# Kernel optimization log

Measured on AMD Instinct MI355X. Metric: run time of the kernel, lower is better.

The kernel has to match this reference:

```python
import jax, jax.numpy as jnp
import numpy as np

N = 8192      # atoms
E = 4096      # edges (become transformer tokens)
E2 = 65536    # edges of second graph y
VOCAB = 119
DE = 200      # node_features == embedding_dim
D = 256
H = 8
L = 2
DFF = 2048


def _bn(x, g, b, eps=1e-6):
    m = x.mean(0)
    v = x.var(0)
    return (x - m) * jax.lax.rsqrt(v + eps) * g + b


def _ln(x, g, b, eps=1e-5):
    m = x.mean(-1, keepdims=True)
    v = ((x - m) ** 2).mean(-1, keepdims=True)
    return (x - m) * jax.lax.rsqrt(v + eps) * g + b


def _gcn(x, ei, W, b):
    # PyG GCNConv: add self loops, symmetric deg^-1/2 normalization
    n = x.shape[0]
    loop = jnp.arange(n)
    src = jnp.concatenate([ei[0], loop])
    dst = jnp.concatenate([ei[1], loop])
    deg = jax.ops.segment_sum(jnp.ones(src.shape[0], x.dtype), dst, num_segments=n)
    dinv = jnp.where(deg > 0, jax.lax.rsqrt(jnp.maximum(deg, 1e-12)), 0.0)
    msg = (x @ W)[src] * (dinv[src] * dinv[dst])[:, None]
    return jax.ops.segment_sum(msg, dst, num_segments=n) + b


def _mha(x, wi, bi, wo, bo):
    S, d = x.shape
    dh = d // H
    q, k, v = jnp.split(x @ wi + bi, 3, axis=1)
    q = q.reshape(S, H, dh)
    k = k.reshape(S, H, dh)
    v = v.reshape(S, H, dh)
    sc = jnp.einsum('qhd,khd->hqk', q, k) * (1.0 / np.sqrt(dh))
    a = jax.nn.softmax(sc, axis=-1)
    o = jnp.einsum('hqk,khd->qhd', a, v).reshape(S, d)
    return o @ wo + bo


def setup_inputs() -> dict:
    key = jax.random.key(0)
    ks = iter(jax.random.split(key, 64))
    nrm = lambda shape, s=0.05: jax.random.normal(next(ks), shape, jnp.float32) * s
    d = {}
    d['x'] = jax.random.randint(next(ks), (N,), 0, VOCAB)
    d['edge_index'] = jax.random.randint(next(ks), (2, E), 1, N + 1)  # 1-based, code subtracts 1
    d['pos'] = jax.random.normal(next(ks), (N, 3), jnp.float32)
    d['y'] = jax.random.randint(next(ks), (2, E2), 0, E)
    d['emb'] = nrm((VOCAB, DE), 1.0)
    d['fc1_w'] = nrm((1, DE))
    d['fc1_b'] = jnp.zeros((DE,), jnp.float32)
    d['bn4_g'] = jnp.ones((DE,), jnp.float32)
    d['bn4_b'] = jnp.zeros((DE,), jnp.float32)
    d['conv1_w'] = nrm((DE, D))
    d['conv1_b'] = jnp.zeros((D,), jnp.float32)
    d['conv2_w'] = nrm((D, D))
    d['conv2_b'] = jnp.zeros((D,), jnp.float32)
    for i in (1, 2, 3):
        d['bn%d_g' % i] = jnp.ones((D,), jnp.float32)
        d['bn%d_b' % i] = jnp.zeros((D,), jnp.float32)
    d['in_proj_w'] = nrm((L, D, 3 * D))
    d['in_proj_b'] = jnp.zeros((L, 3 * D), jnp.float32)
    d['out_proj_w'] = nrm((L, D, D))
    d['out_proj_b'] = jnp.zeros((L, D), jnp.float32)
    d['ln1_g'] = jnp.ones((L, D), jnp.float32)
    d['ln1_b'] = jnp.zeros((L, D), jnp.float32)
    d['ln2_g'] = jnp.ones((L, D), jnp.float32)
    d['ln2_b'] = jnp.zeros((L, D), jnp.float32)
    d['ff1_w'] = nrm((L, D, DFF))
    d['ff1_b'] = jnp.zeros((L, DFF), jnp.float32)
    d['ff2_w'] = nrm((L, DFF, D))
    d['ff2_b'] = jnp.zeros((L, D), jnp.float32)
    d['fc3_w'] = nrm((D, 1))
    d['fc3_b'] = jnp.zeros((1,), jnp.float32)
    d['fc4_w'] = nrm((D, 9))
    d['fc4_b'] = jnp.zeros((9,), jnp.float32)
    return d


def reference(x, edge_index, pos, y, emb, fc1_w, fc1_b, bn4_g, bn4_b,
              conv1_w, conv1_b, conv2_w, conv2_b,
              bn1_g, bn1_b, bn2_g, bn2_b, bn3_g, bn3_b,
              in_proj_w, in_proj_b, out_proj_w, out_proj_b,
              ln1_g, ln1_b, ln2_g, ln2_b, ff1_w, ff1_b, ff2_w, ff2_b,
              fc3_w, fc3_b, fc4_w, fc4_b):
    h = emb[x]                                   # [N, DE]
    ei = edge_index - 1
    row, col = ei[0], ei[1]
    ef = jnp.linalg.norm(pos[col] - pos[row], axis=1, keepdims=True)  # [E,1]
    ef = _bn(ef @ fc1_w + fc1_b, bn4_g, bn4_b)   # [E, DE]
    h = h[row] + h[col] + ef                     # [E, DE] edges -> tokens
    h = jax.nn.leaky_relu(_gcn(h, y, conv1_w, conv1_b))
    h = _bn(h, bn1_g, bn1_b)
    h = jax.nn.leaky_relu(h + _gcn(h, y, conv2_w, conv2_b))
    h = _bn(h, bn2_g, bn2_b)
    # post-norm TransformerEncoder (unbatched seq of length E), dropout=0
    for i in range(L):
        h = _ln(h + _mha(h, in_proj_w[i], in_proj_b[i], out_proj_w[i], out_proj_b[i]),
                ln1_g[i], ln1_b[i])
        ff = jax.nn.relu(h @ ff1_w[i] + ff1_b[i]) @ ff2_w[i] + ff2_b[i]
        h = _ln(h + ff, ln2_g[i], ln2_b[i])
    h = jax.nn.leaky_relu(h)
    h = _bn(h, bn3_g, bn3_b)
    sym_out = h @ fc3_w + fc3_b
    asym_out = h @ fc4_w + fc4_b
    return (sym_out, asym_out)
```

## Files before the change

kernel.cpp:

```cpp
#include <hip/hip_runtime.h>
#include <math.h>

#define ETOK 4096
#define NE2  65536
#define DEF  200
#define DM   256
#define NH   8
#define DH   32
#define DFFN 2048
#define NKS  4

#define QSCALE_LOG2E 0.25503474f

typedef __attribute__((ext_vector_type(8))) short bfrag8;
typedef __attribute__((ext_vector_type(4))) float f32x4;
typedef __attribute__((ext_vector_type(4))) short short4v;

__device__ __forceinline__ unsigned short f2bf(float f) {
  union { float f; unsigned u; } v; v.f = f;
  unsigned u = v.u + 0x7fffu + ((v.u >> 16) & 1u);
  return (unsigned short)(u >> 16);
}
__device__ __forceinline__ float bf2f(unsigned short u) {
  union { unsigned u; float f; } v;
  v.u = ((unsigned)u) << 16;
  return v.f;
}
__device__ __forceinline__ unsigned cvt_pk_bf16(float lo, float hi) {
  unsigned r;
  asm("v_cvt_pk_bf16_f32 %0, %1, %2" : "=v"(r) : "v"(lo), "v"(hi));
  return r;
}

__device__ __forceinline__ float wave_sum(float v) {
#pragma unroll
  for (int off = 32; off > 0; off >>= 1) v += __shfl_xor(v, off);
  return v;
}
__device__ __forceinline__ float block_sum(float v, float* red) {
  v = wave_sum(v);
  int lane = threadIdx.x & 63, w = threadIdx.x >> 6;
  if (lane == 0) red[w] = v;
  __syncthreads();
  float t = red[0] + red[1] + red[2] + red[3];
  __syncthreads();
  return t;
}

__global__ void edge_deg_kernel(const int* __restrict__ ei, const float* __restrict__ pos,
                                float* __restrict__ ef0, float* __restrict__ stats,
                                const int* __restrict__ y, int* __restrict__ deg) {
  __shared__ float red[4];
  int e2 = blockIdx.x * 256 + threadIdx.x;
  atomicAdd(&deg[y[NE2 + e2]], 1);
  if (blockIdx.x < 16) {
    int e = blockIdx.x * 256 + threadIdx.x;
    int r = ei[e] - 1;
    int c = ei[ETOK + e] - 1;
    float dx = pos[c * 3 + 0] - pos[r * 3 + 0];
    float dy = pos[c * 3 + 1] - pos[r * 3 + 1];
    float dz = pos[c * 3 + 2] - pos[r * 3 + 2];
    float d = sqrtf(dx * dx + dy * dy + dz * dz);
    ef0[e] = d;
    float s = block_sum(d, red);
    float s2 = block_sum(d * d, red);
    if (threadIdx.x == 0) {
      atomicAdd(stats + 0, s);
      atomicAdd(stats + 1, s2);
    }
  }
}

__global__ void token_build_kernel(const int* __restrict__ x, const int* __restrict__ ei,
                                   const float* __restrict__ emb, const float* __restrict__ fc1_w,
                                   const float* __restrict__ bn4_g, const float* __restrict__ bn4_b,
                                   const float* __restrict__ ef0, const float* __restrict__ stats,
                                   unsigned short* __restrict__ tokbf) {
  int e = blockIdx.x;
  int j = threadIdx.x;
  float m = stats[0] * (1.0f / 4096.0f);
  float v = stats[1] * (1.0f / 4096.0f) - m * m;
  int xr = x[ei[e] - 1];
  int xc = x[ei[ETOK + e] - 1];
  float dd = ef0[e] - m;
  float val = 0.f;
  if (j < DEF) {
    float w = fc1_w[j];
    float s = w * rsqrtf(v * w * w + 1e-6f) * bn4_g[j];
    val = emb[(size_t)xr * DEF + j] + emb[(size_t)xc * DEF + j] + dd * s + bn4_b[j];
  }
  tokbf[(size_t)e * 256 + j] = f2bf(val);
}

__global__ void scan_kernel(const int* __restrict__ deg, int* __restrict__ off,
                            int* __restrict__ cursor, float* __restrict__ dinv) {
  __shared__ int part[256];
  int t = threadIdx.x;
  int v[16];
  int s = 0;
#pragma unroll
  for (int i = 0; i < 16; ++i) {
    v[i] = deg[t * 16 + i];
    s += v[i];
  }
  part[t] = s;
  __syncthreads();
  if (t == 0) {
    int a = 0;
#pragma unroll 1
    for (int i = 0; i < 256; ++i) {
      int tmp = part[i];
      part[i] = a;
      a += tmp;
    }
    off[4096] = a;
  }
  __syncthreads();
  int a = part[t];
#pragma unroll
  for (int i = 0; i < 16; ++i) {
    off[t * 16 + i] = a;
    cursor[t * 16 + i] = a;
    dinv[t * 16 + i] = rsqrtf((float)(v[i] + 1));
    a += v[i];
  }
}
__global__ void fill_kernel(const int* __restrict__ y, int* __restrict__ cursor,
                            int* __restrict__ srcl) {
  int e = blockIdx.x * 256 + threadIdx.x;
  int s = y[e];
  int d = y[NE2 + e];
  int slot = atomicAdd(&cursor[d], 1);
  srcl[slot] = s;
}

template <int RES, int ACT>
__global__ __launch_bounds__(256) void gather_kernel(const float* __restrict__ xw,
                                                     const int* __restrict__ off,
                                                     const int* __restrict__ srcl,
                                                     const float* __restrict__ dinv,
                                                     const float* __restrict__ bias,
                                                     const float* __restrict__ resid,
                                                     float* __restrict__ out) {
  __shared__ int slds[256];
  __shared__ float dlds[256];
  const int d = blockIdx.x;
  const int c = threadIdx.x;
  const int b0 = off[d], b1 = off[d + 1];
  const float dd = dinv[d];
  float acc = 0.f;
  for (int base = b0; base < b1; base += 256) {
    int n = min(256, b1 - base);
    __syncthreads();
    if (c < n) {
      int s = srcl[base + c];
      slds[c] = s;
      dlds[c] = dinv[s];
    }
    __syncthreads();
    for (int j = 0; j < n; ++j) {
      int s = slds[j];
      acc = fmaf(xw[(size_t)s * DM + c], dlds[j], acc);
    }
  }
  size_t idx = (size_t)d * DM + c;
  float v = bias[c] + xw[idx] * dd * dd + acc * dd;
  if (RES) v += resid[idx];
  if (ACT) v = v > 0.f ? v : 0.01f * v;
  out[idx] = v;
}

struct WEntry {
  const float* src;
  unsigned short* dst;
  int K, N, KP, tilesN, ntiles;
};
struct WPack {
  WEntry e[10];
};
__global__ __launch_bounds__(256) void wtrans_all_kernel(WPack p) {
  __shared__ float tl[32][33];
  int t = blockIdx.x;
  int i = 0;
  while (t >= p.e[i].ntiles) {
    t -= p.e[i].ntiles;
    ++i;
  }
  const WEntry w = p.e[i];
  int nb = (t % w.tilesN) * 32;
  int kb = (t / w.tilesN) * 32;
  int tx = threadIdx.x & 31, ty = threadIdx.x >> 5;
#pragma unroll
  for (int r = ty; r < 32; r += 8) {
    int k = kb + r, n = nb + tx;
    tl[r][tx] = (k < w.K && n < w.N) ? w.src[(size_t)k * w.N + n] : 0.f;
  }
  __syncthreads();
#pragma unroll
  for (int r = ty; r < 32; r += 8) {
    int n = nb + r, k = kb + tx;
    if (n < w.N) w.dst[(size_t)n * w.KP + k] = f2bf(tl[tx][r]);
  }
}

template <int BM, int BN, int OUTBF, int ACT, int QS>
__global__ __launch_bounds__(256) void mfma_gemm(const unsigned short* __restrict__ A,
                                                 const unsigned short* __restrict__ Bt,
                                                 const float* __restrict__ bias,
                                                 void* __restrict__ Cout, int M, int N, int K) {
  constexpr int BK = 64;
  constexpr int TM = BM / 32, TN = BN / 32;
  constexpr int ACH = BM / 32, BCH = BN / 32;
  __shared__ unsigned short Alds[BM * BK];
  __shared__ unsigned short Blds[BN * BK];
  const int tid = threadIdx.x;
  const int lane = tid & 63, wid = tid >> 6;
  const int g = lane >> 4, q = lane & 15;
  const int wr = wid >> 1, wc = wid & 1;
  const int m0 = blockIdx.y * BM, n0 = blockIdx.x * BN;

  f32x4 acc[TM][TN];
#pragma unroll
  for (int i = 0; i < TM; ++i)
#pragma unroll
    for (int j = 0; j < TN; ++j) acc[i][j] = (f32x4){0.f, 0.f, 0.f, 0.f};

  for (int k0 = 0; k0 < K; k0 += BK) {
    __syncthreads();
#pragma unroll
    for (int c = 0; c < ACH; ++c) {
      int chunk = wid * ACH + c;
      int row = chunk * 8 + (lane >> 3);
      int cb = ((lane & 7) * 16) ^ ((row & 7) << 4);
      const char* gp = (const char*)A + ((size_t)(m0 + row) * K + k0) * 2 + cb;
      __builtin_amdgcn_global_load_lds(
          (const __attribute__((address_space(1))) unsigned int*)gp,
          (__attribute__((address_space(3))) unsigned int*)(Alds + chunk * 512), 16, 0, 0);
    }
#pragma unroll
    for (int c = 0; c < BCH; ++c) {
      int chunk = wid * BCH + c;
      int row = chunk * 8 + (lane >> 3);
      int cb = ((lane & 7) * 16) ^ ((row & 7) << 4);
      const char* gp = (const char*)Bt + ((size_t)(n0 + row) * K + k0) * 2 + cb;
      __builtin_amdgcn_global_load_lds(
          (const __attribute__((address_space(1))) unsigned int*)gp,
          (__attribute__((address_space(3))) unsigned int*)(Blds + chunk * 512), 16, 0, 0);
    }
    __syncthreads();
#pragma unroll
    for (int ks = 0; ks < 2; ++ks) {
      bfrag8 af[TM], bfr[TN];
#pragma unroll
      for (int mi = 0; mi < TM; ++mi) {
        int row = wr * (BM / 2) + mi * 16 + q;
        int cb = (ks * 64 + g * 16) ^ ((row & 7) << 4);
        af[mi] = *(const bfrag8*)((const char*)Alds + row * 128 + cb);
      }
#pragma unroll
      for (int ni = 0; ni < TN; ++ni) {
        int row = wc * (BN / 2) + ni * 16 + q;
        int cb = (ks * 64 + g * 16) ^ ((row & 7) << 4);
        bfr[ni] = *(const bfrag8*)((const char*)Blds + row * 128 + cb);
      }
#pragma unroll
      for (int mi = 0; mi < TM; ++mi)
#pragma unroll
        for (int ni = 0; ni < TN; ++ni)
          acc[mi][ni] = __builtin_amdgcn_mfma_f32_16x16x32_bf16(af[mi], bfr[ni], acc[mi][ni], 0, 0, 0);
    }
  }
#pragma unroll
  for (int mi = 0; mi < TM; ++mi) {
    int row = m0 + wr * (BM / 2) + mi * 16 + g * 4;
#pragma unroll
    for (int ni = 0; ni < TN; ++ni) {
      int col = n0 + wc * (BN / 2) + ni * 16 + q;
      float bv = bias ? bias[col] : 0.f;
#pragma unroll
      for (int r = 0; r < 4; ++r) {
        float v = acc[mi][ni][r] + bv;
        if (QS && col < DM) v *= QSCALE_LOG2E;
        if (ACT == 1) v = fmaxf(v, 0.f);
        if (OUTBF)
          ((unsigned short*)Cout)[(size_t)(row + r) * N + col] = f2bf(v);
        else
          ((float*)Cout)[(size_t)(row + r) * N + col] = v;
      }
    }
  }
}

template <int LEAKY>
__global__ __launch_bounds__(256) void col_accum_kernel(const float* __restrict__ x,
                                                        float* __restrict__ colm,
                                                        float* __restrict__ colv) {
  int c = threadIdx.x;
  int r0 = blockIdx.x * 16;
  float s = 0.f, s2 = 0.f;
#pragma unroll
  for (int i = 0; i < 16; ++i) {
    float v = x[(size_t)(r0 + i) * DM + c];
    if (LEAKY) v = v > 0.f ? v : 0.01f * v;
    s += v;
    s2 += v * v;
  }
  atomicAdd(&colm[c], s);
  atomicAdd(&colv[c], s2);
}
template <int LEAKY>
__global__ void bn_apply_kernel(const float* __restrict__ x, const float* __restrict__ colm,
                                const float* __restrict__ colv, const float* __restrict__ g,
                                const float* __restrict__ b, float* __restrict__ outf,
                                unsigned short* __restrict__ outb, int C) {
  size_t i = (size_t)blockIdx.x * 256 + threadIdx.x;
  int c = (int)(i % C);
  float mean = colm[c] * (1.0f / 4096.0f);
  float var = colv[c] * (1.0f / 4096.0f) - mean * mean;
  float v0 = x[i];
  if (LEAKY) v0 = v0 > 0.f ? v0 : 0.01f * v0;
  float v = (v0 - mean) * rsqrtf(var + 1e-6f) * g[c] + b[c];
  outf[i] = v;
  if (outb) outb[i] = f2bf(v);
}

__global__ __launch_bounds__(256) void attn_mfma_kernel(const unsigned short* __restrict__ qkv,
                                                        unsigned short* __restrict__ Opart,
                                                        float* __restrict__ Lpart) {
  const int h = blockIdx.y;
  const int qblk = blockIdx.x * 64;
  const int chunk = blockIdx.z;
  const int tid = threadIdx.x;
  const int wid = tid >> 6, lane = tid & 63;
  const int g = lane >> 4, q = lane & 15;

  __shared__ unsigned short Klds[2][64][40];
  __shared__ unsigned int Vtw[2][32][36];
  __shared__ unsigned short Plds[4][16][72];

  bfrag8 qfrag;
  {
    const unsigned short* qp = qkv + (size_t)(qblk + wid * 16 + q) * 768 + h * DH + g * 8;
    qfrag = *(const bfrag8*)qp;
  }
  const f32x4 zero = {0.f, 0.f, 0.f, 0.f};

  const int skey = tid >> 2;
  const int sdb = (tid & 3) * 8;
  const int kp2 = tid >> 3;
  const int dc = (tid & 7) * 4;

  const int kbeg = chunk * (ETOK / NKS);
  const int NT = (ETOK / NKS) / 64;

  const unsigned short* kptr = qkv + (size_t)(kbeg + skey) * 768 + DM + h * DH + sdb;
  const unsigned short* vptr = qkv + (size_t)(kbeg + kp2 * 2) * 768 + 2 * DM + h * DH + dc;

  bfrag8 kreg = *(const bfrag8*)kptr;
  kptr += 64 * 768;
  short4v va = *(const short4v*)vptr;
  short4v vb = *(const short4v*)(vptr + 768);
  vptr += 64 * 768;

  float lsum = 0.f;
  f32x4 o0 = zero, o1 = zero;

  for (int t = 0; t < NT; ++t) {
    const int buf = t & 1;
    *(bfrag8*)&Klds[buf][skey][sdb] = kreg;
#pragma unroll
    for (int j = 0; j < 4; ++j) {
      unsigned pkv = (unsigned)(unsigned short)va[j] | ((unsigned)(unsigned short)vb[j] << 16);
      Vtw[buf][dc + j][kp2] = pkv;
    }
    __syncthreads();
    if (t + 1 < NT) {
      kreg = *(const bfrag8*)kptr;
      kptr += 64 * 768;
      va = *(const short4v*)vptr;
      vb = *(const short4v*)(vptr + 768);
      vptr += 64 * 768;
    }

    f32x4 st[4];
    __builtin_amdgcn_s_setprio(1);
#pragma unroll
    for (int tt = 0; tt < 4; ++tt) {
      bfrag8 kf = *(const bfrag8*)&Klds[buf][tt * 16 + q][g * 8];
      st[tt] = __builtin_amdgcn_mfma_f32_16x16x32_bf16(kf, qfrag, zero, 0, 0, 0);
    }
    __builtin_amdgcn_s_setprio(0);

    float ps = 0.f;
    unsigned pk8[8];
#pragma unroll
    for (int tt = 0; tt < 4; ++tt) {
      float p0 = __builtin_exp2f(st[tt][0]);
      float p1 = __builtin_exp2f(st[tt][1]);
      float p2 = __builtin_exp2f(st[tt][2]);
      float p3 = __builtin_exp2f(st[tt][3]);
      ps += (p0 + p1) + (p2 + p3);
      pk8[tt * 2 + 0] = cvt_pk_bf16(p0, p1);
      pk8[tt * 2 + 1] = cvt_pk_bf16(p2, p3);
    }
    lsum += ps;

#pragma unroll
    for (int tt = 0; tt < 4; ++tt) {
      uint2 w2;
      w2.x = pk8[tt * 2 + 0];
      w2.y = pk8[tt * 2 + 1];
      *(uint2*)&Plds[wid][q][tt * 16 + g * 4] = w2;
    }

    __builtin_amdgcn_s_setprio(1);
#pragma unroll
    for (int kg = 0; kg < 2; ++kg) {
      bfrag8 pa = *(const bfrag8*)&Plds[wid][q][kg * 32 + g * 8];
      bfrag8 vb0 = *(const bfrag8*)&Vtw[buf][q][kg * 16 + g * 4];
      bfrag8 vb1 = *(const bfrag8*)&Vtw[buf][16 + q][kg * 16 + g * 4];
      o0 = __builtin_amdgcn_mfma_f32_16x16x32_bf16(pa, vb0, o0, 0, 0, 0);
      o1 = __builtin_amdgcn_mfma_f32_16x16x32_bf16(pa, vb1, o1, 0, 0, 0);
    }
    __builtin_amdgcn_s_setprio(0);
  }

  lsum += __shfl_xor(lsum, 16);
  lsum += __shfl_xor(lsum, 32);
#pragma unroll
  for (int r = 0; r < 4; ++r) {
    int row = qblk + wid * 16 + g * 4 + r;
    unsigned short* op = Opart + ((size_t)chunk * ETOK + row) * DM + h * DH;
    op[q] = f2bf(o0[r]);
    op[16 + q] = f2bf(o1[r]);
  }
  if (lane < 16) {
    int row = qblk + wid * 16 + lane;
    Lpart[((size_t)chunk * ETOK + row) * NH + h] = lsum;
  }
}

__global__ __launch_bounds__(256) void attn_combine_kernel(const unsigned short* __restrict__ Opart,
                                                           const float* __restrict__ Lpart,
                                                           unsigned short* __restrict__ out) {
  __shared__ float ls[NKS][NH];
  const int row = blockIdx.x;
  const int c = threadIdx.x;
  if (c < NKS * NH) {
    ls[c >> 3][c & 7] = Lpart[((size_t)(c >> 3) * ETOK + row) * NH + (c & 7)];
  }
  __syncthreads();
  const int h = c >> 5;
  float lstar = (ls[0][h] + ls[1][h]) + (ls[2][h] + ls[3][h]);
  float acc = 0.f;
#pragma unroll
  for (int ch = 0; ch < NKS; ++ch)
    acc += bf2f(Opart[((size_t)ch * ETOK + row) * DM + c]);
  out[(size_t)row * DM + c] = f2bf(acc / lstar);
}

__global__ void add_ln_kernel(const float* __restrict__ x, const float* __restrict__ r,
                              float* __restrict__ outf, unsigned short* __restrict__ outb,
                              const float* __restrict__ g, const float* __restrict__ b) {
  __shared__ float red[4];
  int row = blockIdx.x, t = threadIdx.x;
  size_t idx = (size_t)row * DM + t;
  float v = x[idx] + r[idx];
  float mean = block_sum(v, red) * (1.0f / 256.0f);
  float dv = v - mean;
  float var = block_sum(dv * dv, red) * (1.0f / 256.0f);
  float o = dv * rsqrtf(var + 1e-5f) * g[t] + b[t];
  outf[idx] = o;
  outb[idx] = f2bf(o);
}

__global__ void head_kernel(const float* __restrict__ h, const float* __restrict__ colm,
                            const float* __restrict__ colv, const float* __restrict__ bng,
                            const float* __restrict__ bnb, const float* __restrict__ fc3w,
                            const float* __restrict__ fc3b, const float* __restrict__ fc4w,
                            const float* __restrict__ fc4b, float* __restrict__ out) {
  int wave = threadIdx.x >> 6, lane = threadIdx.x & 63;
  int tok = blockIdx.x * 4 + wave;
  const float* hr = h + (size_t)tok * DM;
  float hv[4];
#pragma unroll
  for (int i = 0; i < 4; ++i) {
    int col = lane * 4 + i;
    float v = hr[col];
    v = v > 0.f ? v : 0.01f * v;
    float mean = colm[col] * (1.0f / 4096.0f);
    float var = colv[col] * (1.0f / 4096.0f) - mean * mean;
    hv[i] = (v - mean) * rsqrtf(var + 1e-6f) * bng[col] + bnb[col];
  }
  float acc = 0.f;
#pragma unroll
  for (int i = 0; i < 4; ++i) acc += hv[i] * fc3w[lane * 4 + i];
  acc = wave_sum(acc);
  if (lane == 0) out[tok] = acc + fc3b[0];
#pragma unroll
  for (int j = 0; j < 9; ++j) {
    float a = 0.f;
#pragma unroll
    for (int i = 0; i < 4; ++i) a += hv[i] * fc4w[(lane * 4 + i) * 9 + j];
    a = wave_sum(a);
    if (lane == 0) out[ETOK + (size_t)tok * 9 + j] = a + fc4b[j];
  }
}

extern "C" void kernel_launch(void* const* d_in, const int* in_sizes, int n_in,
                              void* d_out, int out_size, void* d_ws, size_t ws_size,
                              hipStream_t stream) {
  const int* x = (const int*)d_in[0];
  const int* edge_index = (const int*)d_in[1];
  const float* pos = (const float*)d_in[2];
  const int* y = (const int*)d_in[3];
  const float* emb = (const float*)d_in[4];
  const float* fc1_w = (const float*)d_in[5];
  const float* bn4_g = (const float*)d_in[7];
  const float* bn4_b = (const float*)d_in[8];
  const float* conv1_w = (const float*)d_in[9];
  const float* conv1_b = (const float*)d_in[10];
  const float* conv2_w = (const float*)d_in[11];
  const float* conv2_b = (const float*)d_in[12];
  const float* bn1_g = (const float*)d_in[13];
  const float* bn1_b = (const float*)d_in[14];
  const float* bn2_g = (const float*)d_in[15];
  const float* bn2_b = (const float*)d_in[16];
  const float* bn3_g = (const float*)d_in[17];
  const float* bn3_b = (const float*)d_in[18];
  const float* ipw = (const float*)d_in[19];
  const float* ipb = (const float*)d_in[20];
  const float* opw = (const float*)d_in[21];
  const float* opb = (const float*)d_in[22];
  const float* ln1_g = (const float*)d_in[23];
  const float* ln1_b = (const float*)d_in[24];
  const float* ln2_g = (const float*)d_in[25];
  const float* ln2_b = (const float*)d_in[26];
  const float* ff1w = (const float*)d_in[27];
  const float* ff1b = (const float*)d_in[28];
  const float* ff2w = (const float*)d_in[29];
  const float* ff2b = (const float*)d_in[30];
  const float* fc3w = (const float*)d_in[31];
  const float* fc3b = (const float*)d_in[32];
  const float* fc4w = (const float*)d_in[33];
  const float* fc4b = (const float*)d_in[34];
  float* outp = (float*)d_out;

  char* wsp = (char*)d_ws;
  auto alloc = [&](size_t bytes) {
    void* p = (void*)wsp;
    wsp += (bytes + 255) & ~(size_t)255;
    return p;
  };
  unsigned short* big_bf = (unsigned short*)alloc((size_t)ETOK * DFFN * 2);
  unsigned short* attno = (unsigned short*)alloc((size_t)ETOK * DM * 2);
  unsigned short* h_bf = (unsigned short*)alloc((size_t)ETOK * DM * 2);
  unsigned short* tok_bf = (unsigned short*)alloc((size_t)ETOK * 256 * 2);
  float* hf = (float*)alloc((size_t)ETOK * DM * 4);
  float* t1 = (float*)alloc((size_t)ETOK * DM * 4);
  float* t2 = (float*)alloc((size_t)ETOK * DM * 4);
  unsigned short* Opart = (unsigned short*)alloc((size_t)NKS * ETOK * DM * 2);
  float* Lpart = (float*)alloc((size_t)NKS * ETOK * NH * 4);
  unsigned short* c1wt = (unsigned short*)alloc(256 * 256 * 2);
  unsigned short* c2wt = (unsigned short*)alloc(256 * 256 * 2);
  unsigned short* ipwt = (unsigned short*)alloc((size_t)2 * 768 * 256 * 2);
  unsigned short* opwt = (unsigned short*)alloc((size_t)2 * 256 * 256 * 2);
  unsigned short* f1wt = (unsigned short*)alloc((size_t)2 * 2048 * 256 * 2);
  unsigned short* f2wt = (unsigned short*)alloc((size_t)2 * 256 * 2048 * 2);
  float* ef0 = (float*)alloc(ETOK * 4);
  float* dinv = (float*)alloc(ETOK * 4);
  int* off = (int*)alloc((ETOK + 1) * 4);
  int* cursor = (int*)alloc(ETOK * 4);
  int* srcl = (int*)alloc(NE2 * 4);
  char* z0 = wsp;
  float* stats = (float*)alloc(8 * 4);
  float* colm = (float*)alloc(3 * DM * 4);
  float* colv = (float*)alloc(3 * DM * 4);
  int* deg = (int*)alloc(ETOK * 4);
  size_t zlen = (char*)wsp - z0;

  hipMemsetAsync(z0, 0, zlen, stream);

  WPack wp;
  int ntot = 0;
  auto went = [&](int i, const float* src, unsigned short* dst, int K, int N, int KP) {
    wp.e[i].src = src;
    wp.e[i].dst = dst;
    wp.e[i].K = K;
    wp.e[i].N = N;
    wp.e[i].KP = KP;
    wp.e[i].tilesN = (N + 31) / 32;
    wp.e[i].ntiles = ((N + 31) / 32) * (KP / 32);
    ntot += wp.e[i].ntiles;
  };
  went(0, conv1_w, c1wt, 200, 256, 256);
  went(1, conv2_w, c2wt, 256, 256, 256);
  went(2, ipw, ipwt, 256, 768, 256);
  went(3, ipw + (size_t)256 * 768, ipwt + (size_t)768 * 256, 256, 768, 256);
  went(4, opw, opwt, 256, 256, 256);
  went(5, opw + (size_t)256 * 256, opwt + (size_t)256 * 256, 256, 256, 256);
  went(6, ff1w, f1wt, 256, 2048, 256);
  went(7, ff1w + (size_t)256 * 2048, f1wt + (size_t)2048 * 256, 256, 2048, 256);
  went(8, ff2w, f2wt, 2048, 256, 2048);
  went(9, ff2w + (size_t)2048 * 256, f2wt + (size_t)256 * 2048, 2048, 256, 2048);
  wtrans_all_kernel<<<ntot, 256, 0, stream>>>(wp);

  edge_deg_kernel<<<NE2 / 256, 256, 0, stream>>>(edge_index, pos, ef0, stats, y, deg);
  scan_kernel<<<1, 256, 0, stream>>>(deg, off, cursor, dinv);
  fill_kernel<<<NE2 / 256, 256, 0, stream>>>(y, cursor, srcl);
  token_build_kernel<<<ETOK, 256, 0, stream>>>(x, edge_index, emb, fc1_w, bn4_g, bn4_b, ef0,
                                               stats, tok_bf);

  mfma_gemm<32, 32, 0, 0, 0><<<dim3(8, 128), 256, 0, stream>>>(tok_bf, c1wt, nullptr, t1, ETOK, DM, 256);
  gather_kernel<0, 1><<<ETOK, 256, 0, stream>>>(t1, off, srcl, dinv, conv1_b, nullptr, t2);
  col_accum_kernel<0><<<ETOK / 16, 256, 0, stream>>>(t2, colm, colv);
  bn_apply_kernel<0><<<ETOK * DM / 256, 256, 0, stream>>>(t2, colm, colv, bn1_g, bn1_b, hf, h_bf, DM);

  mfma_gemm<32, 32, 0, 0, 0><<<dim3(8, 128), 256, 0, stream>>>(h_bf, c2wt, nullptr, t1, ETOK, DM, 256);
  gather_kernel<1, 1><<<ETOK, 256, 0, stream>>>(t1, off, srcl, dinv, conv2_b, hf, t2);
  col_accum_kernel<0><<<ETOK / 16, 256, 0, stream>>>(t2, colm + DM, colv + DM);
  bn_apply_kernel<0><<<ETOK * DM / 256, 256, 0, stream>>>(t2, colm + DM, colv + DM, bn2_g, bn2_b,
                                                          hf, h_bf, DM);

  for (int i = 0; i < 2; ++i) {
    mfma_gemm<32, 32, 1, 0, 1><<<dim3(24, 128), 256, 0, stream>>>(
        h_bf, ipwt + (size_t)i * 768 * 256, ipb + (size_t)i * 768, big_bf, ETOK, 768, 256);
    attn_mfma_kernel<<<dim3(ETOK / 64, NH, NKS), 256, 0, stream>>>(big_bf, Opart, Lpart);
    attn_combine_kernel<<<ETOK, 256, 0, stream>>>(Opart, Lpart, attno);
    mfma_gemm<32, 32, 0, 0, 0><<<dim3(8, 128), 256, 0, stream>>>(
        attno, opwt + (size_t)i * 256 * 256, opb + (size_t)i * DM, t2, ETOK, DM, 256);
    add_ln_kernel<<<ETOK, 256, 0, stream>>>(t2, hf, hf, h_bf, ln1_g + (size_t)i * DM,
                                            ln1_b + (size_t)i * DM);
    mfma_gemm<64, 64, 1, 1, 0><<<dim3(32, 64), 256, 0, stream>>>(
        h_bf, f1wt + (size_t)i * 2048 * 256, ff1b + (size_t)i * DFFN, big_bf, ETOK, DFFN, 256);
    mfma_gemm<32, 32, 0, 0, 0><<<dim3(8, 128), 256, 0, stream>>>(
        big_bf, f2wt + (size_t)i * 256 * 2048, ff2b + (size_t)i * DM, t2, ETOK, DM, 2048);
    add_ln_kernel<<<ETOK, 256, 0, stream>>>(t2, hf, hf, h_bf, ln2_g + (size_t)i * DM,
                                            ln2_b + (size_t)i * DM);
  }

  col_accum_kernel<1><<<ETOK / 16, 256, 0, stream>>>(hf, colm + 2 * DM, colv + 2 * DM);
  head_kernel<<<ETOK / 4, 256, 0, stream>>>(hf, colm + 2 * DM, colv + 2 * DM, bn3_g, bn3_b,
                                            fc3w, fc3b, fc4w, fc4b, outp);
}
```

Measured before the change: 343.8 us.

## Write V transposed from QKV GEMM and process 32 queries per wave in attention

The QKV projection GEMM now writes Q and K into a 512-wide buffer and V into a separate transposed buffer (head-dim major, token minor). The attention kernel can then load V tiles with a single 16-byte vector store to LDS instead of packing pairs of rows. Each wave also handles 32 query rows instead of 16, so every K/V tile staged in LDS is reused twice and half as many blocks are launched. The cost is more registers per thread (launch_bounds 256,4), a larger P buffer in LDS, and scattered 8-byte transposed stores in the GEMM epilogue.

```diff
diff --git a/kernel.cpp b/kernel.cpp
--- a/kernel.cpp
+++ b/kernel.cpp
@@ -15,6 +15,7 @@
 typedef __attribute__((ext_vector_type(8))) short bfrag8;
 typedef __attribute__((ext_vector_type(4))) float f32x4;
 typedef __attribute__((ext_vector_type(4))) short short4v;
+typedef __attribute__((ext_vector_type(4))) unsigned int u32x4;
 
 __device__ __forceinline__ unsigned short f2bf(float f) {
   union { float f; unsigned u; } v; v.f = f;
@@ -203,11 +204,12 @@
   }
 }
 
-template <int BM, int BN, int OUTBF, int ACT, int QS>
+template <int BM, int BN, int OUTBF, int ACT, int QS, int VSPLIT>
 __global__ __launch_bounds__(256) void mfma_gemm(const unsigned short* __restrict__ A,
                                                  const unsigned short* __restrict__ Bt,
                                                  const float* __restrict__ bias,
-                                                 void* __restrict__ Cout, int M, int N, int K) {
+                                                 void* __restrict__ Cout, void* __restrict__ Cout2,
+                                                 int M, int N, int K) {
   constexpr int BK = 64;
   constexpr int TM = BM / 32, TN = BN / 32;
   constexpr int ACH = BM / 32, BCH = BN / 32;
@@ -277,15 +279,22 @@
     for (int ni = 0; ni < TN; ++ni) {
       int col = n0 + wc * (BN / 2) + ni * 16 + q;
       float bv = bias ? bias[col] : 0.f;
-#pragma unroll
-      for (int r = 0; r < 4; ++r) {
-        float v = acc[mi][ni][r] + bv;
-        if (QS && col < DM) v *= QSCALE_LOG2E;
-        if (ACT == 1) v = fmaxf(v, 0.f);
-        if (OUTBF)
-          ((unsigned short*)Cout)[(size_t)(row + r) * N + col] = f2bf(v);
-        else
-          ((float*)Cout)[(size_t)(row + r) * N + col] = v;
+      if (VSPLIT && col >= 512) {
+        short4v pkv;
+#pragma unroll
+        for (int r = 0; r < 4; ++r) pkv[r] = (short)f2bf(acc[mi][ni][r] + bv);
+        *(short4v*)((unsigned short*)Cout2 + (size_t)(col - 512) * M + row) = pkv;
+      } else {
+#pragma unroll
+        for (int r = 0; r < 4; ++r) {
+          float v = acc[mi][ni][r] + bv;
+          if (QS && col < DM) v *= QSCALE_LOG2E;
+          if (ACT == 1) v = fmaxf(v, 0.f);
+          if (OUTBF)
+            ((unsigned short*)Cout)[(size_t)(row + r) * (VSPLIT ? 512 : N) + col] = f2bf(v);
+          else
+            ((float*)Cout)[(size_t)(row + r) * N + col] = v;
+        }
       }
     }
   }
@@ -324,11 +333,12 @@
   if (outb) outb[i] = f2bf(v);
 }
 
-__global__ __launch_bounds__(256) void attn_mfma_kernel(const unsigned short* __restrict__ qkv,
-                                                        unsigned short* __restrict__ Opart,
-                                                        float* __restrict__ Lpart) {
+__global__ __launch_bounds__(256, 4) void attn_mfma_kernel(const unsigned short* __restrict__ qk,
+                                                           const unsigned short* __restrict__ vt,
+                                                           unsigned short* __restrict__ Opart,
+                                                           float* __restrict__ Lpart) {
   const int h = blockIdx.y;
-  const int qblk = blockIdx.x * 64;
+  const int qblk = blockIdx.x * 128;
   const int chunk = blockIdx.z;
   const int tid = threadIdx.x;
   const int wid = tid >> 6, lane = tid & 63;
@@ -336,107 +346,123 @@
 
   __shared__ unsigned short Klds[2][64][40];
   __shared__ unsigned int Vtw[2][32][36];
-  __shared__ unsigned short Plds[4][16][72];
-
-  bfrag8 qfrag;
+  __shared__ unsigned short Plds[4][32][72];
+
+  bfrag8 qfrag0, qfrag1;
   {
-    const unsigned short* qp = qkv + (size_t)(qblk + wid * 16 + q) * 768 + h * DH + g * 8;
-    qfrag = *(const bfrag8*)qp;
+    const unsigned short* qp = qk + (size_t)(qblk + wid * 32 + q) * 512 + h * DH + g * 8;
+    qfrag0 = *(const bfrag8*)qp;
+    qfrag1 = *(const bfrag8*)(qp + 16 * 512);
   }
   const f32x4 zero = {0.f, 0.f, 0.f, 0.f};
 
   const int skey = tid >> 2;
   const int sdb = (tid & 3) * 8;
-  const int kp2 = tid >> 3;
-  const int dc = (tid & 7) * 4;
+  const int sd = tid >> 3;
+  const int sk4 = (tid & 7) * 4;
 
   const int kbeg = chunk * (ETOK / NKS);
   const int NT = (ETOK / NKS) / 64;
 
-  const unsigned short* kptr = qkv + (size_t)(kbeg + skey) * 768 + DM + h * DH + sdb;
-  const unsigned short* vptr = qkv + (size_t)(kbeg + kp2 * 2) * 768 + 2 * DM + h * DH + dc;
+  const unsigned short* kptr = qk + (size_t)(kbeg + skey) * 512 + DM + h * DH + sdb;
+  const unsigned short* vptr = vt + (size_t)(h * DH + sd) * ETOK + kbeg + sk4 * 2;
 
   bfrag8 kreg = *(const bfrag8*)kptr;
-  kptr += 64 * 768;
-  short4v va = *(const short4v*)vptr;
-  short4v vb = *(const short4v*)(vptr + 768);
-  vptr += 64 * 768;
-
-  float lsum = 0.f;
-  f32x4 o0 = zero, o1 = zero;
+  kptr += (size_t)64 * 512;
+  u32x4 vreg = *(const u32x4*)vptr;
+  vptr += 64;
+
+  float lsum0 = 0.f, lsum1 = 0.f;
+  f32x4 o00 = zero, o01 = zero, o10 = zero, o11 = zero;
 
   for (int t = 0; t < NT; ++t) {
     const int buf = t & 1;
     *(bfrag8*)&Klds[buf][skey][sdb] = kreg;
-#pragma unroll
-    for (int j = 0; j < 4; ++j) {
-      unsigned pkv = (unsigned)(unsigned short)va[j] | ((unsigned)(unsigned short)vb[j] << 16);
-      Vtw[buf][dc + j][kp2] = pkv;
-    }
+    *(u32x4*)&Vtw[buf][sd][sk4] = vreg;
     __syncthreads();
     if (t + 1 < NT) {
       kreg = *(const bfrag8*)kptr;
-      kptr += 64 * 768;
-      va = *(const short4v*)vptr;
-      vb = *(const short4v*)(vptr + 768);
-      vptr += 64 * 768;
-    }
-
-    f32x4 st[4];
+      kptr += (size_t)64 * 512;
+      vreg = *(const u32x4*)vptr;
+      vptr += 64;
+    }
+
+    f32x4 st0[4], st1[4];
     __builtin_amdgcn_s_setprio(1);
 #pragma unroll
     for (int tt = 0; tt < 4; ++tt) {
       bfrag8 kf = *(const bfrag8*)&Klds[buf][tt * 16 + q][g * 8];
-      st[tt] = __builtin_amdgcn_mfma_f32_16x16x32_bf16(kf, qfrag, zero, 0, 0, 0);
+      st0[tt] = __builtin_amdgcn_mfma_f32_16x16x32_bf16(kf, qfrag0, zero, 0, 0, 0);
+      st1[tt] = __builtin_amdgcn_mfma_f32_16x16x32_bf16(kf, qfrag1, zero, 0, 0, 0);
     }
     __builtin_amdgcn_s_setprio(0);
 
-    float ps = 0.f;
-    unsigned pk8[8];
-#pragma unroll
-    for (int tt = 0; tt < 4; ++tt) {
-      float p0 = __builtin_exp2f(st[tt][0]);
-      float p1 = __builtin_exp2f(st[tt][1]);
-      float p2 = __builtin_exp2f(st[tt][2]);
-      float p3 = __builtin_exp2f(st[tt][3]);
-      ps += (p0 + p1) + (p2 + p3);
-      pk8[tt * 2 + 0] = cvt_pk_bf16(p0, p1);
-      pk8[tt * 2 + 1] = cvt_pk_bf16(p2, p3);
-    }
-    lsum += ps;
-
-#pragma unroll
-    for (int tt = 0; tt < 4; ++tt) {
-      uint2 w2;
-      w2.x = pk8[tt * 2 + 0];
-      w2.y = pk8[tt * 2 + 1];
-      *(uint2*)&Plds[wid][q][tt * 16 + g * 4] = w2;
+    {
+      float ps = 0.f;
+#pragma unroll
+      for (int tt = 0; tt < 4; ++tt) {
+        float p0 = __builtin_exp2f(st0[tt][0]);
+        float p1 = __builtin_exp2f(st0[tt][1]);
+        float p2 = __builtin_exp2f(st0[tt][2]);
+        float p3 = __builtin_exp2f(st0[tt][3]);
+        ps += (p0 + p1) + (p2 + p3);
+        uint2 w2;
+        w2.x = cvt_pk_bf16(p0, p1);
+        w2.y = cvt_pk_bf16(p2, p3);
+        *(uint2*)&Plds[wid][q][tt * 16 + g * 4] = w2;
+      }
+      lsum0 += ps;
+    }
+    {
+      float ps = 0.f;
+#pragma unroll
+      for (int tt = 0; tt < 4; ++tt) {
+        float p0 = __builtin_exp2f(st1[tt][0]);
+        float p1 = __builtin_exp2f(st1[tt][1]);
+        float p2 = __builtin_exp2f(st1[tt][2]);
+        float p3 = __builtin_exp2f(st1[tt][3]);
+        ps += (p0 + p1) + (p2 + p3);
+        uint2 w2;
+        w2.x = cvt_pk_bf16(p0, p1);
+        w2.y = cvt_pk_bf16(p2, p3);
+        *(uint2*)&Plds[wid][16 + q][tt * 16 + g * 4] = w2;
+      }
+      lsum1 += ps;
     }
 
     __builtin_amdgcn_s_setprio(1);
 #pragma unroll
     for (int kg = 0; kg < 2; ++kg) {
-      bfrag8 pa = *(const bfrag8*)&Plds[wid][q][kg * 32 + g * 8];
       bfrag8 vb0 = *(const bfrag8*)&Vtw[buf][q][kg * 16 + g * 4];
       bfrag8 vb1 = *(const bfrag8*)&Vtw[buf][16 + q][kg * 16 + g * 4];
-      o0 = __builtin_amdgcn_mfma_f32_16x16x32_bf16(pa, vb0, o0, 0, 0, 0);
-      o1 = __builtin_amdgcn_mfma_f32_16x16x32_bf16(pa, vb1, o1, 0, 0, 0);
+      bfrag8 pa0 = *(const bfrag8*)&Plds[wid][q][kg * 32 + g * 8];
+      bfrag8 pa1 = *(const bfrag8*)&Plds[wid][16 + q][kg * 32 + g * 8];
+      o00 = __builtin_amdgcn_mfma_f32_16x16x32_bf16(pa0, vb0, o00, 0, 0, 0);
+      o01 = __builtin_amdgcn_mfma_f32_16x16x32_bf16(pa0, vb1, o01, 0, 0, 0);
+      o10 = __builtin_amdgcn_mfma_f32_16x16x32_bf16(pa1, vb0, o10, 0, 0, 0);
+      o11 = __builtin_amdgcn_mfma_f32_16x16x32_bf16(pa1, vb1, o11, 0, 0, 0);
     }
     __builtin_amdgcn_s_setprio(0);
   }
 
-  lsum += __shfl_xor(lsum, 16);
-  lsum += __shfl_xor(lsum, 32);
+  lsum0 += __shfl_xor(lsum0, 16);
+  lsum0 += __shfl_xor(lsum0, 32);
+  lsum1 += __shfl_xor(lsum1, 16);
+  lsum1 += __shfl_xor(lsum1, 32);
 #pragma unroll
   for (int r = 0; r < 4; ++r) {
-    int row = qblk + wid * 16 + g * 4 + r;
-    unsigned short* op = Opart + ((size_t)chunk * ETOK + row) * DM + h * DH;
-    op[q] = f2bf(o0[r]);
-    op[16 + q] = f2bf(o1[r]);
+    int row0 = qblk + wid * 32 + g * 4 + r;
+    unsigned short* op0 = Opart + ((size_t)chunk * ETOK + row0) * DM + h * DH;
+    op0[q] = f2bf(o00[r]);
+    op0[16 + q] = f2bf(o01[r]);
+    unsigned short* op1 = op0 + (size_t)16 * DM;
+    op1[q] = f2bf(o10[r]);
+    op1[16 + q] = f2bf(o11[r]);
   }
   if (lane < 16) {
-    int row = qblk + wid * 16 + lane;
-    Lpart[((size_t)chunk * ETOK + row) * NH + h] = lsum;
+    int row = qblk + wid * 32 + lane;
+    Lpart[((size_t)chunk * ETOK + row) * NH + h] = lsum0;
+    Lpart[((size_t)chunk * ETOK + row + 16) * NH + h] = lsum1;
   }
 }
 
@@ -553,6 +579,8 @@
     return p;
   };
   unsigned short* big_bf = (unsigned short*)alloc((size_t)ETOK * DFFN * 2);
+  unsigned short* qk_bf = (unsigned short*)alloc((size_t)ETOK * 512 * 2);
+  unsigned short* vt_bf = (unsigned short*)alloc((size_t)DM * ETOK * 2);
   unsigned short* attno = (unsigned short*)alloc((size_t)ETOK * DM * 2);
   unsigned short* h_bf = (unsigned short*)alloc((size_t)ETOK * DM * 2);
   unsigned short* tok_bf = (unsigned short*)alloc((size_t)ETOK * 256 * 2);
@@ -611,30 +639,32 @@
   token_build_kernel<<<ETOK, 256, 0, stream>>>(x, edge_index, emb, fc1_w, bn4_g, bn4_b, ef0,
                                                stats, tok_bf);
 
-  mfma_gemm<32, 32, 0, 0, 0><<<dim3(8, 128), 256, 0, stream>>>(tok_bf, c1wt, nullptr, t1, ETOK, DM, 256);
+  mfma_gemm<32, 32, 0, 0, 0, 0><<<dim3(8, 128), 256, 0, stream>>>(tok_bf, c1wt, nullptr, t1,
+                                                                  nullptr, ETOK, DM, 256);
   gather_kernel<0, 1><<<ETOK, 256, 0, stream>>>(t1, off, srcl, dinv, conv1_b, nullptr, t2);
   col_accum_kernel<0><<<ETOK / 16, 256, 0, stream>>>(t2, colm, colv);
   bn_apply_kernel<0><<<ETOK * DM / 256, 256, 0, stream>>>(t2, colm, colv, bn1_g, bn1_b, hf, h_bf, DM);
 
-  mfma_gemm<32, 32, 0, 0, 0><<<dim3(8, 128), 256, 0, stream>>>(h_bf, c2wt, nullptr, t1, ETOK, DM, 256);
+  mfma_gemm<32, 32, 0, 0, 0, 0><<<dim3(8, 128), 256, 0, stream>>>(h_bf, c2wt, nullptr, t1,
+                                                                  nullptr, ETOK, DM, 256);
   gather_kernel<1, 1><<<ETOK, 256, 0, stream>>>(t1, off, srcl, dinv, conv2_b, hf, t2);
   col_accum_kernel<0><<<ETOK / 16, 256, 0, stream>>>(t2, colm + DM, colv + DM);
   bn_apply_kernel<0><<<ETOK * DM / 256, 256, 0, stream>>>(t2, colm + DM, colv + DM, bn2_g, bn2_b,
                                                           hf, h_bf, DM);
 
   for (int i = 0; i < 2; ++i) {
-    mfma_gemm<32, 32, 1, 0, 1><<<dim3(24, 128), 256, 0, stream>>>(
-        h_bf, ipwt + (size_t)i * 768 * 256, ipb + (size_t)i * 768, big_bf, ETOK, 768, 256);
-    attn_mfma_kernel<<<dim3(ETOK / 64, NH, NKS), 256, 0, stream>>>(big_bf, Opart, Lpart);
+    mfma_gemm<32, 32, 1, 0, 1, 1><<<dim3(24, 128), 256, 0, stream>>>(
+        h_bf, ipwt + (size_t)i * 768 * 256, ipb + (size_t)i * 768, qk_bf, vt_bf, ETOK, 768, 256);
+    attn_mfma_kernel<<<dim3(ETOK / 128, NH, NKS), 256, 0, stream>>>(qk_bf, vt_bf, Opart, Lpart);
     attn_combine_kernel<<<ETOK, 256, 0, stream>>>(Opart, Lpart, attno);
-    mfma_gemm<32, 32, 0, 0, 0><<<dim3(8, 128), 256, 0, stream>>>(
-        attno, opwt + (size_t)i * 256 * 256, opb + (size_t)i * DM, t2, ETOK, DM, 256);
+    mfma_gemm<32, 32, 0, 0, 0, 0><<<dim3(8, 128), 256, 0, stream>>>(
+        attno, opwt + (size_t)i * 256 * 256, opb + (size_t)i * DM, t2, nullptr, ETOK, DM, 256);
     add_ln_kernel<<<ETOK, 256, 0, stream>>>(t2, hf, hf, h_bf, ln1_g + (size_t)i * DM,
                                             ln1_b + (size_t)i * DM);
-    mfma_gemm<64, 64, 1, 1, 0><<<dim3(32, 64), 256, 0, stream>>>(
-        h_bf, f1wt + (size_t)i * 2048 * 256, ff1b + (size_t)i * DFFN, big_bf, ETOK, DFFN, 256);
-    mfma_gemm<32, 32, 0, 0, 0><<<dim3(8, 128), 256, 0, stream>>>(
-        big_bf, f2wt + (size_t)i * 256 * 2048, ff2b + (size_t)i * DM, t2, ETOK, DM, 2048);
+    mfma_gemm<64, 64, 1, 1, 0, 0><<<dim3(32, 64), 256, 0, stream>>>(
+        h_bf, f1wt + (size_t)i * 2048 * 256, ff1b + (size_t)i * DFFN, big_bf, nullptr, ETOK, DFFN, 256);
+    mfma_gemm<32, 32, 0, 0, 0, 0><<<dim3(8, 128), 256, 0, stream>>>(
+        big_bf, f2wt + (size_t)i * 256 * 2048, ff2b + (size_t)i * DM, t2, nullptr, ETOK, DM, 2048);
     add_ln_kernel<<<ETOK, 256, 0, stream>>>(t2, hf, hf, h_bf, ln2_g + (size_t)i * DM,
                                             ln2_b + (size_t)i * DM);
   }
```

Result: faster. 327.8 us (-4.6%).
